# Kernel optimization log

Measured on AMD Instinct MI355X. Metric: run time of the kernel, lower is better.

## Reference

```python
import jax, jax.numpy as jnp
import numpy as np
from functools import partial

# Straight-through sign (Binarize): sign forward, identity gradient
@jax.custom_vjp
def ste_sign(x):
    return jnp.sign(x)

def _ste_fwd(x):
    return jnp.sign(x), None

def _ste_bwd(_, g):
    return (g,)

ste_sign.defvjp(_ste_fwd, _ste_bwd)


def conv2d(x, w):
    # x: [N,C,H,W], w: [O,I,kh,kw], VALID conv, stride 1
    return jax.lax.conv_general_dilated(
        x, w, window_strides=(1, 1), padding='VALID',
        dimension_numbers=('NCHW', 'OIHW', 'NCHW'))


def maxpool2x2(x):
    return jax.lax.reduce_window(
        x, -jnp.inf, jax.lax.max, (1, 1, 2, 2), (1, 1, 2, 2), 'VALID')


def setup_inputs() -> dict:
    key = jax.random.key(0)
    ks = jax.random.split(key, 32)
    d = {}
    d['x'] = jax.random.normal(ks[0], (128, 3, 32, 32), dtype=jnp.float32)
    wshapes = [(128, 3, 3, 3), (128, 128, 3, 3), (256, 128, 3, 3),
               (256, 256, 3, 3), (512, 256, 3, 3), (512, 512, 3, 3),
               (10, 512, 4, 4)]
    for i, s in enumerate(wshapes):
        d[f'w{i+1}'] = jax.random.normal(ks[1 + i], s, dtype=jnp.float32) * 0.05
    bn_ch = [128, 128, 256, 256, 512, 512, 10]
    for i, c in enumerate(bn_ch):
        d[f'bn{i+1}_s'] = jax.random.uniform(ks[10 + 2 * i], (c,), dtype=jnp.float32,
                                             minval=0.5, maxval=1.5)
        d[f'bn{i+1}_t'] = jax.random.normal(ks[11 + 2 * i], (c,), dtype=jnp.float32) * 0.1
    return d


def _forward(x, w1, w2, w3, w4, w5, w6, w7,
             bn1_s, bn1_t, bn2_s, bn2_t, bn3_s, bn3_t, bn4_s, bn4_t,
             bn5_s, bn5_t, bn6_s, bn6_t, bn7_s, bn7_t):
    def block(h, w, s, t, pool, binarize_in):
        if binarize_in:
            h = ste_sign(h)            # binarize activations (in_ch != 3)
        h = jnp.pad(h, ((0, 0), (0, 0), (1, 1), (1, 1)))  # F.pad value=0
        h = conv2d(h, ste_sign(w))      # binarized weights
        if pool:
            h = maxpool2x2(h)
        h = h * s[None, :, None, None] + t[None, :, None, None]  # eval BN
        return jnp.clip(h, -1.0, 1.0)   # Hardtanh

    h = block(x, w1, bn1_s, bn1_t, pool=False, binarize_in=False)  # 32x32x128
    h = block(h, w2, bn2_s, bn2_t, pool=True,  binarize_in=True)   # 16x16x128
    h = block(h, w3, bn3_s, bn3_t, pool=False, binarize_in=True)   # 16x16x256
    h = block(h, w4, bn4_s, bn4_t, pool=True,  binarize_in=True)   # 8x8x256
    h = block(h, w5, bn5_s, bn5_t, pool=False, binarize_in=True)   # 8x8x512
    h = block(h, w6, bn6_s, bn6_t, pool=True,  binarize_in=True)   # 4x4x512
    # conv7: binarize input + weights, 4x4 kernel, no padding -> [N,10,1,1]
    h = conv2d(ste_sign(h), ste_sign(w7))
    h = h.reshape(-1, 10)
    h = h * bn7_s + bn7_t               # eval BatchNorm1d(10)
    return jax.nn.log_softmax(h, axis=1)


def reference(x, w1, w2, w3, w4, w5, w6, w7,
              bn1_s, bn1_t, bn2_s, bn2_t, bn3_s, bn3_t, bn4_s, bn4_t,
              bn5_s, bn5_t, bn6_s, bn6_t, bn7_s, bn7_t):
    return _forward(x, w1, w2, w3, w4, w5, w6, w7,
                    bn1_s, bn1_t, bn2_s, bn2_t, bn3_s, bn3_t, bn4_s, bn4_t,
                    bn5_s, bn5_t, bn6_s, bn6_t, bn7_s, bn7_t)
```

## Files before the change

### kernel.cpp

```cpp
#include <hip/hip_runtime.h>
#include <cstdint>
#include <math.h>

#define NB 128

__global__ void pack_all_kernel(
    const float* __restrict__ w1,
    const float* __restrict__ w2, const float* __restrict__ w3,
    const float* __restrict__ w4, const float* __restrict__ w5,
    const float* __restrict__ w6, const float* __restrict__ w7,
    uint32_t* __restrict__ wp1,
    uint32_t* __restrict__ wp2, uint32_t* __restrict__ wp3,
    uint32_t* __restrict__ wp4, uint32_t* __restrict__ wp5,
    uint32_t* __restrict__ wp6, uint32_t* __restrict__ wp7) {
  int i = blockIdx.x * 256 + threadIdx.x;
  if (i >= 145516) return;
  if (i >= 145408) {
    int j = i - 145408;
    int ocg = j / 54, rem = j % 54, t = rem >> 1, half = rem & 1;
    uint32_t word = 0;
    for (int b = 0; b < 32; ++b)
      word |= ((w1[(ocg * 64 + half * 32 + b) * 27 + t] >= 0.0f) ? 1u : 0u) << b;
    wp1[(ocg * 27 + t) * 2 + half] = word;
    return;
  }
  const float* w; uint32_t* wp; int C, KHW; bool nl = true;
  if (i < 4608)        { w = w2; wp = wp2; C = 128; KHW = 9; }
  else if (i < 13824)  { i -= 4608;   w = w3; wp = wp3; C = 128; KHW = 9; }
  else if (i < 32256)  { i -= 13824;  w = w4; wp = wp4; C = 256; KHW = 9; }
  else if (i < 69120)  { i -= 32256;  w = w5; wp = wp5; C = 256; KHW = 9; }
  else if (i < 142848) { i -= 69120;  w = w6; wp = wp6; C = 512; KHW = 9; }
  else                 { i -= 142848; w = w7; wp = wp7; C = 512; KHW = 16; nl = false; }
  int Cw = C >> 5;
  int cw = i % Cw;
  int rest = i / Cw;
  int t = rest % KHW;
  int o = rest / KHW;
  uint32_t word = 0;
  for (int b = 0; b < 32; ++b)
    word |= ((w[(o * C + cw * 32 + b) * KHW + t] >= 0.0f) ? 1u : 0u) << b;
  if (nl) wp[(((o >> 6) * KHW + t) * Cw + cw) * 64 + (o & 63)] = word;
  else    wp[(o * KHW + t) * Cw + cw] = word;
}

__device__ __forceinline__ bool lane_bit(uint64_t m, int lane) {
#if __has_builtin(__builtin_amdgcn_inverse_ballot_w64)
  (void)lane;
  return __builtin_amdgcn_inverse_ballot_w64(m);
#else
  return (m >> lane) & 1;
#endif
}

template <int PC, int R>
__global__ __launch_bounds__(64, 6) void conv1_kernel(
    const float* __restrict__ x, const uint32_t* __restrict__ wp1,
    const float* __restrict__ bs, const float* __restrict__ bt,
    uint32_t* __restrict__ out) {
  const int lane = threadIdx.x;
  const int ocg = blockIdx.y;
  const int cpr = 32 / PC;
  const int c = blockIdx.x;
  const int cg = c % cpr;
  const int rg = (c / cpr) % (32 / R);
  const int n  = c / (cpr * (32 / R));
  const int y0 = rg * R, x0 = cg * PC;

  double acc[R * PC];
#pragma unroll
  for (int p = 0; p < R * PC; ++p) acc[p] = 0.0;

  const uint64_t* wm64 = (const uint64_t*)wp1;
  for (int ic = 0; ic < 3; ++ic) {
    uint64_t wm[9];
#pragma unroll
    for (int t = 0; t < 9; ++t) wm[t] = wm64[ocg * 27 + ic * 9 + t];
#pragma unroll
    for (int ey = -1; ey <= R; ++ey) {
      const int y = y0 + ey;
      if (y < 0 || y >= 32) continue;
#pragma unroll
      for (int ex = -1; ex <= PC; ++ex) {
        const int xx = x0 + ex;
        if (xx < 0 || xx >= 32) continue;
        const double xd = (double)x[((n * 3 + ic) * 32 + y) * 32 + xx];
#pragma unroll
        for (int r = 0; r < R; ++r) {
          const int kh = ey - r + 1;
          if (kh < 0 || kh > 2) continue;
#pragma unroll
          for (int kw = 0; kw < 3; ++kw) {
            const int pxo = ex - kw + 1;
            if (pxo < 0 || pxo >= PC) continue;
            const bool neg = lane_bit(wm[kh * 3 + kw], lane) == false;
            acc[r * PC + pxo] += neg ? -xd : xd;
          }
        }
      }
    }
  }

  const double sd = (double)bs[ocg * 64 + lane];
  const double td = (double)bt[ocg * 64 + lane];
  uint64_t bal[R * PC];
#pragma unroll
  for (int r = 0; r < R; ++r)
#pragma unroll
    for (int pxo = 0; pxo < PC; ++pxo) {
      double v = acc[r * PC + pxo] * sd + td;
      bal[r * PC + pxo] = __ballot(v >= 0.0);
    }
  if (lane == 0) {
#pragma unroll
    for (int r = 0; r < R; ++r)
#pragma unroll
      for (int pxo = 0; pxo < PC; ++pxo) {
        const int p = ((n * 32 + (y0 + r)) * 32 + (x0 + pxo));
        uint32_t* o = out + p * 4 + ocg * 2;
        uint64_t m = bal[r * PC + pxo];
        o[0] = (uint32_t)m; o[1] = (uint32_t)(m >> 32);
      }
  }
}

template <int CW, int CWP, int H, int W, int PC, int R, bool POOL, int MINW>
__global__ __launch_bounds__(64, MINW) void bconv_kernel(
    const uint32_t* __restrict__ act, const uint32_t* __restrict__ wpk,
    const float* __restrict__ bs, const float* __restrict__ bt,
    uint32_t* __restrict__ out, int OCW) {
  static_assert(CW % CWP == 0, "");
  const int lane = threadIdx.x;
  const int ocg = blockIdx.y;
  const int cpr = W / PC;
  const int c = blockIdx.x;
  const int cg = c % cpr;
  const int rg = (c / cpr) % (H / R);
  const int n  = c / (cpr * (H / R));
  const int y0 = rg * R, x0 = cg * PC;

  int acc[R * PC];
#pragma unroll
  for (int p = 0; p < R * PC; ++p) acc[p] = 0;

#pragma unroll
  for (int pass = 0; pass < CW / CWP; ++pass) {
    uint32_t wreg[9 * CWP];
#pragma unroll
    for (int t = 0; t < 9; ++t)
#pragma unroll
      for (int cw = 0; cw < CWP; ++cw)
        wreg[t * CWP + cw] = wpk[(((ocg * 9) + t) * CW + pass * CWP + cw) * 64 + lane];

#pragma unroll
    for (int ry = -1; ry <= R; ++ry) {
      const int y = y0 + ry;
      if (y < 0 || y >= H) continue;
#pragma unroll
      for (int cc = -1; cc <= PC; ++cc) {
        const int x = x0 + cc;
        if (x < 0 || x >= W) continue;
        const uint32_t* ap = act + ((n * H + y) * W + x) * CW + pass * CWP;
        uint32_t av[CWP];
#pragma unroll
        for (int cw = 0; cw < CWP; ++cw) av[cw] = ap[cw];
#pragma unroll
        for (int r = 0; r < R; ++r) {
          const int kh = ry - r + 1;
          if (kh < 0 || kh > 2) continue;
#pragma unroll
          for (int kw = 0; kw < 3; ++kw) {
            const int pxo = cc - kw + 1;
            if (pxo < 0 || pxo >= PC) continue;
#pragma unroll
            for (int cw = 0; cw < CWP; ++cw)
              acc[r * PC + pxo] += __popc(av[cw] ^ wreg[(kh * 3 + kw) * CWP + cw]);
          }
        }
      }
    }
  }

  const double sd = (double)bs[ocg * 64 + lane];
  const double td = (double)bt[ocg * 64 + lane];
  if (!POOL) {
    uint64_t bal[R * PC];
#pragma unroll
    for (int r = 0; r < R; ++r)
#pragma unroll
      for (int pxo = 0; pxo < PC; ++pxo) {
        const int y = y0 + r, x = x0 + pxo;
        const int nv = CW * (3 - (y == 0) - (y == H - 1)) * (3 - (x == 0) - (x == W - 1));
        double v = (double)(32 * nv - 2 * acc[r * PC + pxo]) * sd + td;
        bal[r * PC + pxo] = __ballot(v >= 0.0);
      }
    if (lane == 0) {
#pragma unroll
      for (int r = 0; r < R; ++r)
#pragma unroll
        for (int pxo = 0; pxo < PC; ++pxo) {
          uint32_t* o = out + ((n * H + (y0 + r)) * W + (x0 + pxo)) * OCW + ocg * 2;
          uint64_t m = bal[r * PC + pxo];
          o[0] = (uint32_t)m; o[1] = (uint32_t)(m >> 32);
        }
    }
  } else {
    static_assert(!POOL || R == 2, "pool needs row pairs");
    uint64_t pooled[PC / 2];
#pragma unroll
    for (int c2 = 0; c2 < PC / 2; ++c2) pooled[c2] = 0;
#pragma unroll
    for (int r = 0; r < R; ++r)
#pragma unroll
      for (int pxo = 0; pxo < PC; ++pxo) {
        const int y = y0 + r, x = x0 + pxo;
        const int nv = CW * (3 - (y == 0) - (y == H - 1)) * (3 - (x == 0) - (x == W - 1));
        double v = (double)(32 * nv - 2 * acc[r * PC + pxo]) * sd + td;
        pooled[pxo >> 1] |= __ballot(v >= 0.0);
      }
    if (lane == 0) {
#pragma unroll
      for (int c2 = 0; c2 < PC / 2; ++c2) {
        const int yo = y0 >> 1, xo = (x0 >> 1) + c2;
        uint32_t* o = out + ((n * (H / 2) + yo) * (W / 2) + xo) * OCW + ocg * 2;
        o[0] = (uint32_t)pooled[c2]; o[1] = (uint32_t)(pooled[c2] >> 32);
      }
    }
  }
}

__global__ __launch_bounds__(64) void conv7_kernel(
    const uint32_t* __restrict__ act, const uint32_t* __restrict__ wp,
    const float* __restrict__ bs, const float* __restrict__ bt,
    float* __restrict__ out) {
  int n = blockIdx.x;
  int lane = threadIdx.x;
  const uint32_t* a = act + n * 256;
  __shared__ double logits[10];
  for (int o = 0; o < 10; ++o) {
    int acc = 0;
    for (int w = lane; w < 256; w += 64) acc += __popc(a[w] ^ wp[o * 256 + w]);
    for (int off = 32; off > 0; off >>= 1) acc += __shfl_down(acc, off, 64);
    if (lane == 0) {
      double dotd = (double)(8192 - 2 * acc);
      logits[o] = dotd * (double)bs[o] + (double)bt[o];
    }
  }
  __syncthreads();
  if (lane == 0) {
    double m = logits[0];
    for (int o = 1; o < 10; ++o) m = fmax(m, logits[o]);
    double s = 0.0;
    for (int o = 0; o < 10; ++o) s += exp(logits[o] - m);
    double lse = log(s);
    for (int o = 0; o < 10; ++o) out[n * 10 + o] = (float)(logits[o] - m - lse);
  }
}

extern "C" void kernel_launch(void* const* d_in, const int* in_sizes, int n_in,
                              void* d_out, int out_size, void* d_ws, size_t ws_size,
                              hipStream_t stream) {
  const float* x  = (const float*)d_in[0];
  const float* w1 = (const float*)d_in[1];
  const float* w2 = (const float*)d_in[2];
  const float* w3 = (const float*)d_in[3];
  const float* w4 = (const float*)d_in[4];
  const float* w5 = (const float*)d_in[5];
  const float* w6 = (const float*)d_in[6];
  const float* w7 = (const float*)d_in[7];
  const float* s1 = (const float*)d_in[8];  const float* t1 = (const float*)d_in[9];
  const float* s2 = (const float*)d_in[10]; const float* t2 = (const float*)d_in[11];
  const float* s3 = (const float*)d_in[12]; const float* t3 = (const float*)d_in[13];
  const float* s4 = (const float*)d_in[14]; const float* t4 = (const float*)d_in[15];
  const float* s5 = (const float*)d_in[16]; const float* t5 = (const float*)d_in[17];
  const float* s6 = (const float*)d_in[18]; const float* t6 = (const float*)d_in[19];
  const float* s7 = (const float*)d_in[20]; const float* t7 = (const float*)d_in[21];
  float* out = (float*)d_out;

  uint32_t* ws = (uint32_t*)d_ws;
  uint32_t* A   = ws;
  uint32_t* B   = ws + 524288;
  uint32_t* wp2 = ws + 1048576;
  uint32_t* wp3 = wp2 + 4608;
  uint32_t* wp4 = wp3 + 9216;
  uint32_t* wp5 = wp4 + 18432;
  uint32_t* wp6 = wp5 + 36864;
  uint32_t* wp7 = wp6 + 73728;
  uint32_t* wp1 = wp7 + 2560;

  pack_all_kernel<<<dim3(569), dim3(256), 0, stream>>>(
      w1, w2, w3, w4, w5, w6, w7, wp1, wp2, wp3, wp4, wp5, wp6, wp7);

  conv1_kernel<8, 2><<<dim3(8192, 2), dim3(64), 0, stream>>>(x, wp1, s1, t1, A);

  bconv_kernel<4, 4, 32, 32, 8, 2, true, 6>
      <<<dim3(8192, 2), dim3(64), 0, stream>>>(A, wp2, s2, t2, B, 4);

  bconv_kernel<4, 4, 16, 16, 16, 1, false, 6>
      <<<dim3(2048, 4), dim3(64), 0, stream>>>(B, wp3, s3, t3, A, 8);

  bconv_kernel<8, 8, 16, 16, 8, 2, true, 4>
      <<<dim3(2048, 4), dim3(64), 0, stream>>>(A, wp4, s4, t4, B, 8);

  bconv_kernel<8, 8, 8, 8, 8, 2, false, 4>
      <<<dim3(512, 8), dim3(64), 0, stream>>>(B, wp5, s5, t5, A, 16);

  bconv_kernel<16, 8, 8, 8, 8, 2, true, 4>
      <<<dim3(512, 8), dim3(64), 0, stream>>>(A, wp6, s6, t6, B, 16);

  conv7_kernel<<<dim3(128), dim3(64), 0, stream>>>(B, wp7, s7, t7, out);
}
```

Baseline: 322.4 us.

## Use float accumulation in conv1 with fp64 fallback, retune bconv tiles

Conv1 now accumulates in fp32 with FMA against precomputed ±1 sign floats instead of double adds. When the result is close to the sign threshold, the lane recomputes that pixel in double, so the binarized output should still match. Output stores become single 64-bit writes. The bconv launches for layers 3–6 get smaller pixel tiles, a smaller channel chunk and higher occupancy hints. The price is a divergent recompute path and more blocks.

```diff
diff --git a/kernel.cpp b/kernel.cpp
--- a/kernel.cpp
+++ b/kernel.cpp
@@ -66,15 +66,17 @@
   const int n  = c / (cpr * (32 / R));
   const int y0 = rg * R, x0 = cg * PC;
 
-  double acc[R * PC];
-#pragma unroll
-  for (int p = 0; p < R * PC; ++p) acc[p] = 0.0;
-
   const uint64_t* wm64 = (const uint64_t*)wp1;
+  float sgn[27];
+#pragma unroll
+  for (int t = 0; t < 27; ++t)
+    sgn[t] = lane_bit(wm64[ocg * 27 + t], lane) ? 1.0f : -1.0f;
+
+  float acc[R * PC];
+#pragma unroll
+  for (int p = 0; p < R * PC; ++p) acc[p] = 0.0f;
+
   for (int ic = 0; ic < 3; ++ic) {
-    uint64_t wm[9];
-#pragma unroll
-    for (int t = 0; t < 9; ++t) wm[t] = wm64[ocg * 27 + ic * 9 + t];
 #pragma unroll
     for (int ey = -1; ey <= R; ++ey) {
       const int y = y0 + ey;
@@ -83,7 +85,7 @@
       for (int ex = -1; ex <= PC; ++ex) {
         const int xx = x0 + ex;
         if (xx < 0 || xx >= 32) continue;
-        const double xd = (double)x[((n * 3 + ic) * 32 + y) * 32 + xx];
+        const float xv = x[((n * 3 + ic) * 32 + y) * 32 + xx];
 #pragma unroll
         for (int r = 0; r < R; ++r) {
           const int kh = ey - r + 1;
@@ -92,8 +94,7 @@
           for (int kw = 0; kw < 3; ++kw) {
             const int pxo = ex - kw + 1;
             if (pxo < 0 || pxo >= PC) continue;
-            const bool neg = lane_bit(wm[kh * 3 + kw], lane) == false;
-            acc[r * PC + pxo] += neg ? -xd : xd;
+            acc[r * PC + pxo] = fmaf(xv, sgn[ic * 9 + kh * 3 + kw], acc[r * PC + pxo]);
           }
         }
       }
@@ -107,7 +108,26 @@
   for (int r = 0; r < R; ++r)
 #pragma unroll
     for (int pxo = 0; pxo < PC; ++pxo) {
-      double v = acc[r * PC + pxo] * sd + td;
+      double v = (double)acc[r * PC + pxo] * sd + td;
+      const bool risky = fabs(v) < 0.005 * sd;
+      if (__any(risky)) {
+        if (risky) {
+          const int y = y0 + r, xp = x0 + pxo;
+          double ad = 0.0;
+          for (int ic = 0; ic < 3; ++ic)
+            for (int kh = 0; kh < 3; ++kh) {
+              const int yy = y + kh - 1;
+              if ((unsigned)yy >= 32u) continue;
+              for (int kw = 0; kw < 3; ++kw) {
+                const int xc = xp + kw - 1;
+                if ((unsigned)xc >= 32u) continue;
+                const double xd = (double)x[((n * 3 + ic) * 32 + yy) * 32 + xc];
+                ad += (sgn[ic * 9 + kh * 3 + kw] > 0.0f) ? xd : -xd;
+              }
+            }
+          v = ad * sd + td;
+        }
+      }
       bal[r * PC + pxo] = __ballot(v >= 0.0);
     }
   if (lane == 0) {
@@ -116,9 +136,7 @@
 #pragma unroll
       for (int pxo = 0; pxo < PC; ++pxo) {
         const int p = ((n * 32 + (y0 + r)) * 32 + (x0 + pxo));
-        uint32_t* o = out + p * 4 + ocg * 2;
-        uint64_t m = bal[r * PC + pxo];
-        o[0] = (uint32_t)m; o[1] = (uint32_t)(m >> 32);
+        *(uint64_t*)(out + p * 4 + ocg * 2) = bal[r * PC + pxo];
       }
   }
 }
@@ -197,11 +215,9 @@
 #pragma unroll
       for (int r = 0; r < R; ++r)
 #pragma unroll
-        for (int pxo = 0; pxo < PC; ++pxo) {
-          uint32_t* o = out + ((n * H + (y0 + r)) * W + (x0 + pxo)) * OCW + ocg * 2;
-          uint64_t m = bal[r * PC + pxo];
-          o[0] = (uint32_t)m; o[1] = (uint32_t)(m >> 32);
-        }
+        for (int pxo = 0; pxo < PC; ++pxo)
+          *(uint64_t*)(out + ((n * H + (y0 + r)) * W + (x0 + pxo)) * OCW + ocg * 2) =
+              bal[r * PC + pxo];
     }
   } else {
     static_assert(!POOL || R == 2, "pool needs row pairs");
@@ -221,8 +237,8 @@
 #pragma unroll
       for (int c2 = 0; c2 < PC / 2; ++c2) {
         const int yo = y0 >> 1, xo = (x0 >> 1) + c2;
-        uint32_t* o = out + ((n * (H / 2) + yo) * (W / 2) + xo) * OCW + ocg * 2;
-        o[0] = (uint32_t)pooled[c2]; o[1] = (uint32_t)(pooled[c2] >> 32);
+        *(uint64_t*)(out + ((n * (H / 2) + yo) * (W / 2) + xo) * OCW + ocg * 2) =
+            pooled[c2];
       }
     }
   }
@@ -295,17 +311,17 @@
   bconv_kernel<4, 4, 32, 32, 8, 2, true, 6>
       <<<dim3(8192, 2), dim3(64), 0, stream>>>(A, wp2, s2, t2, B, 4);
 
-  bconv_kernel<4, 4, 16, 16, 16, 1, false, 6>
-      <<<dim3(2048, 4), dim3(64), 0, stream>>>(B, wp3, s3, t3, A, 8);
-
-  bconv_kernel<8, 8, 16, 16, 8, 2, true, 4>
+  bconv_kernel<4, 4, 16, 16, 8, 1, false, 6>
+      <<<dim3(4096, 4), dim3(64), 0, stream>>>(B, wp3, s3, t3, A, 8);
+
+  bconv_kernel<8, 4, 16, 16, 8, 2, true, 6>
       <<<dim3(2048, 4), dim3(64), 0, stream>>>(A, wp4, s4, t4, B, 8);
 
-  bconv_kernel<8, 8, 8, 8, 8, 2, false, 4>
-      <<<dim3(512, 8), dim3(64), 0, stream>>>(B, wp5, s5, t5, A, 16);
-
-  bconv_kernel<16, 8, 8, 8, 8, 2, true, 4>
-      <<<dim3(512, 8), dim3(64), 0, stream>>>(A, wp6, s6, t6, B, 16);
+  bconv_kernel<8, 4, 8, 8, 4, 2, false, 6>
+      <<<dim3(1024, 8), dim3(64), 0, stream>>>(B, wp5, s5, t5, A, 16);
+
+  bconv_kernel<16, 4, 8, 8, 4, 2, true, 6>
+      <<<dim3(1024, 8), dim3(64), 0, stream>>>(A, wp6, s6, t6, B, 16);
 
   conv7_kernel<<<dim3(128), dim3(64), 0, stream>>>(B, wp7, s7, t7, out);
 }
```

Result: slower. 364.1 us (+12.9%).
